# Kernel tuning notes

Measured on AMD Instinct MI355X. Metric: run time of the kernel, lower is better.

Reference implementation:

```python
import jax, jax.numpy as jnp
import numpy as np

L = 5        # num_layers
DIM = 128    # data dim
SPLIT = DIM // 2   # 64
H = 64       # hidden_dim (fixed in AffineCouplingLayer)
OUT = DIM - SPLIT  # 64
B = 262144   # batch


def setup_inputs() -> dict:
    key = jax.random.key(0)
    ks = jax.random.split(key, 13)

    def p(k, shape, fan_in):
        return jax.random.normal(k, shape, jnp.float32) * (1.0 / np.sqrt(fan_in))

    inp = {
        "x": jax.random.normal(ks[0], (B, DIM), jnp.float32),
        # s_net params, stacked over layers. Linear stored as [in, out] (y = x @ W + b)
        "s_W1": p(ks[1], (L, SPLIT, H), SPLIT), "s_b1": jnp.zeros((L, H), jnp.float32),
        "s_W2": p(ks[2], (L, H, H), H),         "s_b2": jnp.zeros((L, H), jnp.float32),
        "s_W3": p(ks[3], (L, H, OUT), H),       "s_b3": jnp.zeros((L, OUT), jnp.float32),
        # t_net params
        "t_W1": p(ks[4], (L, SPLIT, H), SPLIT), "t_b1": jnp.zeros((L, H), jnp.float32),
        "t_W2": p(ks[5], (L, H, H), H),         "t_b2": jnp.zeros((L, H), jnp.float32),
        "t_W3": p(ks[6], (L, H, OUT), H),       "t_b3": jnp.zeros((L, OUT), jnp.float32),
    }
    return inp


def _mlp(x0, W1, b1, W2, b2, W3, b3):
    # 3-layer MLP with LeakyReLU(0.01) between layers (torch default slope)
    h = jax.nn.leaky_relu(x0 @ W1 + b1, 0.01)
    h = jax.nn.leaky_relu(h @ W2 + b2, 0.01)
    return h @ W3 + b3


def reference(x, s_W1, s_b1, s_W2, s_b2, s_W3, s_b3,
              t_W1, t_b1, t_W2, t_b2, t_W3, t_b3):
    x0 = x[:, :SPLIT]          # never changes across layers (matches source)
    x1 = x[:, SPLIT:]
    log_det = jnp.zeros(x.shape[0], x.dtype)
    for l in range(L):
        s = jnp.tanh(_mlp(x0, s_W1[l], s_b1[l], s_W2[l], s_b2[l], s_W3[l], s_b3[l]))
        t = _mlp(x0, t_W1[l], t_b1[l], t_W2[l], t_b2[l], t_W3[l], t_b3[l])
        x1 = x1 * jnp.exp(s) + t
        log_det = log_det + jnp.sum(s, axis=1)
    z = jnp.concatenate([x0, x1], axis=1)
    return z, log_det
```

## Files before the change

### kernel.cpp

```cpp
#include <hip/hip_runtime.h>

typedef __fp16 f16;
typedef __fp16 f16x2 __attribute__((ext_vector_type(2)));
typedef __fp16 f16x8 __attribute__((ext_vector_type(8)));
typedef float f32x4 __attribute__((ext_vector_type(4)));
typedef float f32x16 __attribute__((ext_vector_type(16)));

__device__ __forceinline__ unsigned pkrtz(float a, float b) {
    f16x2 r = __builtin_amdgcn_cvt_pkrtz(a, b);
    return __builtin_bit_cast(unsigned, r);
}

__device__ __forceinline__ f16x8 pack4(unsigned a, unsigned b, unsigned c, unsigned d) {
    union { unsigned u[4]; f16x8 v; } r;
    r.u[0] = a; r.u[1] = b; r.u[2] = c; r.u[3] = d;
    return r.v;
}

__global__ __launch_bounds__(512) void pack_w(
    const float* __restrict__ sW1, const float* __restrict__ sW2, const float* __restrict__ sW3,
    const float* __restrict__ tW1, const float* __restrict__ tW2, const float* __restrict__ tW3,
    f16* __restrict__ wp) {
    int mat = blockIdx.x;
    int layer = mat / 6;
    int rem = mat % 6;
    int fi = threadIdx.x >> 6;
    int lane = threadIdx.x & 63;
    int tile = fi >> 2, kt = fi & 3;
    int h = lane >> 5;
    int m = (lane & 31) + 32 * tile;
    const float* Wt[6] = {sW1, sW2, sW3, tW1, tW2, tW3};
    const float* W = Wt[rem] + layer * 4096;
    f16x8 v;
#pragma unroll
    for (int e = 0; e < 8; ++e) {
        int k = 16 * kt + 4 * h + (e & 3) + ((e >> 2) << 3);
        v[e] = (f16)W[k * 64 + m];
    }
    *(f16x8*)(wp + ((size_t)mat * 8 + fi) * 512 + lane * 8) = v;
}

__global__ __launch_bounds__(512) void pack_b(
    const float* __restrict__ sb1, const float* __restrict__ sb2, const float* __restrict__ sb3,
    const float* __restrict__ tb1, const float* __restrict__ tb2, const float* __restrict__ tb3,
    float* __restrict__ wb) {
    int i = blockIdx.x * 512 + threadIdx.x;
    if (i >= 1920) return;
    int l = i / 384, r = i % 384, mat = r / 64, j = r % 64;
    const float* B[6] = {sb1, sb2, sb3, tb1, tb2, tb3};
    wb[l * 384 + mat * 64 + j] = B[mat][l * 64 + j];
}

__device__ __forceinline__ void bias_init(const float* bias, int h, f32x16 c[2]) {
#pragma unroll
    for (int t = 0; t < 2; ++t) {
#pragma unroll
        for (int r4 = 0; r4 < 4; ++r4) {
            f32x4 bb = *(const f32x4*)(bias + 32 * t + 8 * r4 + 4 * h);
            c[t][4 * r4 + 0] = bb[0];
            c[t][4 * r4 + 1] = bb[1];
            c[t][4 * r4 + 2] = bb[2];
            c[t][4 * r4 + 3] = bb[3];
        }
    }
}

__device__ __forceinline__ void gemm1(const f16* w, const f16x8 in[4],
                                      const float* bias, int lane, f32x16 c[2]) {
    const int h = (lane >> 5) & 1;
    bias_init(bias, h, c);
#pragma unroll
    for (int mt = 0; mt < 2; ++mt) {
#pragma unroll
        for (int kt = 0; kt < 4; ++kt) {
            f16x8 wf = *(const f16x8*)(w + (mt * 4 + kt) * 512 + lane * 8);
            c[mt] = __builtin_amdgcn_mfma_f32_32x32x16_f16(wf, in[kt], c[mt], 0, 0, 0);
        }
    }
}

__device__ __forceinline__ void relu_pack(const f32x16 c[2], f16x8 o[4]) {
    const f16 hc = (f16)0.01f;
    const f16x8 c001 = {hc, hc, hc, hc, hc, hc, hc, hc};
#pragma unroll
    for (int kt = 0; kt < 4; ++kt) {
        const int tl = kt >> 1;
        const int base = 8 * (kt & 1);
        f16x8 v = pack4(pkrtz(c[tl][base + 0], c[tl][base + 1]),
                        pkrtz(c[tl][base + 2], c[tl][base + 3]),
                        pkrtz(c[tl][base + 4], c[tl][base + 5]),
                        pkrtz(c[tl][base + 6], c[tl][base + 7]));
        o[kt] = __builtin_elementwise_max(v, v * c001);
    }
}

__device__ __forceinline__ void mlp3(const f16* w, const f16x8 x0f[4],
                                     int lane, f32x16 out[2]) {
    const float* bias = (const float*)(w + 12288);
    f32x16 c1[2];
    gemm1(w, x0f, bias, lane, c1);
    f16x8 h1[4];
    relu_pack(c1, h1);
    f32x16 c2[2];
    gemm1(w + 4096, h1, bias + 64, lane, c2);
    f16x8 h2[4];
    relu_pack(c2, h2);
    gemm1(w + 8192, h2, bias + 128, lane, out);
}

#define SLOT 12672

__global__ __launch_bounds__(512, 2)
void flow_main(const float* __restrict__ x, const f16* __restrict__ wp,
               float* __restrict__ out, int nrows) {
    __shared__ f16 wl[SLOT];
    const int tid = threadIdx.x;
    const int lane = tid & 63;
    const int wv = tid >> 6;
    const int h = lane >> 5;
    const int n = (blockIdx.x * 8 + wv) * 32 + (lane & 31);
    const float* xr = x + (size_t)n * 128;
    float* zr = out + (size_t)n * 128;
    const float* wbias_g = (const float*)((const char*)wp + 491520);

    f32x4 stg0, stg1, stg2;
    f32x4 stgb = {0.f, 0.f, 0.f, 0.f};

    {
        const f32x4* src = (const f32x4*)wp;
        stg0 = src[tid]; stg1 = src[tid + 512]; stg2 = src[tid + 1024];
        f32x4* dst = (f32x4*)wl;
        dst[tid] = stg0; dst[tid + 512] = stg1; dst[tid + 1024] = stg2;
        if (tid < 48) {
            stgb = ((const f32x4*)wbias_g)[tid];
            ((f32x4*)(wl + 12288))[tid] = stgb;
        }
    }

    f16x8 x0f[4];
#pragma unroll
    for (int kt = 0; kt < 4; ++kt) {
        f32x4 a = *(const f32x4*)(xr + 16 * kt + 4 * h);
        f32x4 b = *(const f32x4*)(xr + 16 * kt + 8 + 4 * h);
        *(f32x4*)(zr + 16 * kt + 4 * h) = a;
        *(f32x4*)(zr + 16 * kt + 8 + 4 * h) = b;
        x0f[kt] = pack4(pkrtz(a[0], a[1]), pkrtz(a[2], a[3]), pkrtz(b[0], b[1]), pkrtz(b[2], b[3]));
    }

    f16x8 x1h[4];
#pragma unroll
    for (int i = 0; i < 4; ++i) {
        const int t = i >> 1, q = i & 1;
        f32x4 a = *(const f32x4*)(xr + 64 + 32 * t + 16 * q + 4 * h);
        f32x4 b = *(const f32x4*)(xr + 64 + 32 * t + 16 * q + 8 + 4 * h);
        x1h[i] = pack4(pkrtz(a[0], a[1]), pkrtz(a[2], a[3]),
                       pkrtz(b[0], b[1]), pkrtz(b[2], b[3]));
    }

    __syncthreads();

    float ld = 0.f;
#pragma unroll 1
    for (int l = 0; l < 5; ++l) {
        {
            const f32x4* src = (const f32x4*)(wp + (size_t)l * 24576 + 12288);
            stg0 = src[tid]; stg1 = src[tid + 512]; stg2 = src[tid + 1024];
            if (tid < 48) stgb = ((const f32x4*)(wbias_g + l * 384 + 192))[tid];
        }

        f32x16 cs[2];
        mlp3(wl, x0f, lane, cs);

#pragma unroll
        for (int i = 0; i < 4; ++i) {
            const int t = i >> 1, q = i & 1;
            f16x8 xo = x1h[i];
            float nf[8];
#pragma unroll
            for (int e = 0; e < 8; ++e) {
                float y = cs[t][8 * q + e];
                float u = __builtin_amdgcn_exp2f(2.8853900817779268f * y);
                float rc = __builtin_amdgcn_rcpf(u + 1.f);
                float s = fmaf(-2.f, rc, 1.f);
                ld += s;
                float ef = __builtin_amdgcn_exp2f(fmaf(-2.8853900817779268f, rc, 1.4426950408889634f));
                nf[e] = (float)xo[e] * ef;
            }
            x1h[i] = pack4(pkrtz(nf[0], nf[1]), pkrtz(nf[2], nf[3]),
                           pkrtz(nf[4], nf[5]), pkrtz(nf[6], nf[7]));
        }

        __syncthreads();
        {
            f32x4* dst = (f32x4*)wl;
            dst[tid] = stg0; dst[tid + 512] = stg1; dst[tid + 1024] = stg2;
            if (tid < 48) ((f32x4*)(wl + 12288))[tid] = stgb;
        }
        __syncthreads();

        if (l < 4) {
            const f32x4* src = (const f32x4*)(wp + (size_t)(l + 1) * 24576);
            stg0 = src[tid]; stg1 = src[tid + 512]; stg2 = src[tid + 1024];
            if (tid < 48) stgb = ((const f32x4*)(wbias_g + (l + 1) * 384))[tid];
        }

        f32x16 ct[2];
        mlp3(wl, x0f, lane, ct);

#pragma unroll
        for (int i = 0; i < 4; ++i) {
            const int t = i >> 1, q = i & 1;
            f16x8 xo = x1h[i];
            float nf[8];
#pragma unroll
            for (int e = 0; e < 8; ++e)
                nf[e] = (float)xo[e] + ct[t][8 * q + e];
            x1h[i] = pack4(pkrtz(nf[0], nf[1]), pkrtz(nf[2], nf[3]),
                           pkrtz(nf[4], nf[5]), pkrtz(nf[6], nf[7]));
        }

        if (l < 4) {
            __syncthreads();
            {
                f32x4* dst = (f32x4*)wl;
                dst[tid] = stg0; dst[tid + 512] = stg1; dst[tid + 1024] = stg2;
                if (tid < 48) ((f32x4*)(wl + 12288))[tid] = stgb;
            }
            __syncthreads();
        }
    }

#pragma unroll
    for (int i = 0; i < 4; ++i) {
        const int t = i >> 1, q = i & 1;
        f16x8 v = x1h[i];
        f32x4 a = {(float)v[0], (float)v[1], (float)v[2], (float)v[3]};
        f32x4 b = {(float)v[4], (float)v[5], (float)v[6], (float)v[7]};
        *(f32x4*)(zr + 64 + 32 * t + 16 * q + 4 * h) = a;
        *(f32x4*)(zr + 64 + 32 * t + 16 * q + 8 + 4 * h) = b;
    }

    float tot = ld + __shfl_xor(ld, 32);
    if (h == 0) out[(size_t)nrows * 128 + n] = tot;
}

extern "C" void kernel_launch(void* const* d_in, const int* in_sizes, int n_in,
                              void* d_out, int out_size, void* d_ws, size_t ws_size,
                              hipStream_t stream) {
    const float* x   = (const float*)d_in[0];
    const float* sW1 = (const float*)d_in[1];
    const float* sb1 = (const float*)d_in[2];
    const float* sW2 = (const float*)d_in[3];
    const float* sb2 = (const float*)d_in[4];
    const float* sW3 = (const float*)d_in[5];
    const float* sb3 = (const float*)d_in[6];
    const float* tW1 = (const float*)d_in[7];
    const float* tb1 = (const float*)d_in[8];
    const float* tW2 = (const float*)d_in[9];
    const float* tb2 = (const float*)d_in[10];
    const float* tW3 = (const float*)d_in[11];
    const float* tb3 = (const float*)d_in[12];

    f16* wp = (f16*)d_ws;
    float* wb = (float*)((char*)d_ws + 491520);
    int nrows = in_sizes[0] / 128;

    pack_w<<<30, 512, 0, stream>>>(sW1, sW2, sW3, tW1, tW2, tW3, wp);
    pack_b<<<4, 512, 0, stream>>>(sb1, sb2, sb3, tb1, tb2, tb3, wb);
    flow_main<<<nrows / 256, 512, 0, stream>>>(x, wp, (float*)d_out, nrows);
}
```

Baseline: 139.2 us.

## Double-buffer weight slots in LDS using direct global-to-LDS loads

Register-staged weight copies are replaced by asynchronous global_load_lds transfers into two LDS slots. The next MLP's weights stream into one slot while the current MLP reads the other, which drops one barrier pair per layer half and frees the staging registers. MFMA loops are also wrapped in s_setprio so matrix work gets issue priority. The cost is double the LDS footprint per block, which could limit occupancy, plus reliance on the compiler placing the right waits before each barrier.

```diff
diff --git a/kernel.cpp b/kernel.cpp
--- a/kernel.cpp
+++ b/kernel.cpp
@@ -15,6 +15,12 @@
     union { unsigned u[4]; f16x8 v; } r;
     r.u[0] = a; r.u[1] = b; r.u[2] = c; r.u[3] = d;
     return r.v;
+}
+
+__device__ __forceinline__ void glds16(const void* g, void* l) {
+    __builtin_amdgcn_global_load_lds(
+        (const __attribute__((address_space(1))) unsigned*)g,
+        (__attribute__((address_space(3))) unsigned*)l, 16, 0, 0);
 }
 
 __global__ __launch_bounds__(512) void pack_w(
@@ -69,6 +75,7 @@
                                       const float* bias, int lane, f32x16 c[2]) {
     const int h = (lane >> 5) & 1;
     bias_init(bias, h, c);
+    __builtin_amdgcn_s_setprio(1);
 #pragma unroll
     for (int mt = 0; mt < 2; ++mt) {
 #pragma unroll
@@ -77,6 +84,7 @@
             c[mt] = __builtin_amdgcn_mfma_f32_32x32x16_f16(wf, in[kt], c[mt], 0, 0, 0);
         }
     }
+    __builtin_amdgcn_s_setprio(0);
 }
 
 __device__ __forceinline__ void relu_pack(const f32x16 c[2], f16x8 o[4]) {
@@ -108,12 +116,12 @@
     gemm1(w + 8192, h2, bias + 128, lane, out);
 }
 
-#define SLOT 12672
+#define SLOTB 25344
 
 __global__ __launch_bounds__(512, 2)
 void flow_main(const float* __restrict__ x, const f16* __restrict__ wp,
                float* __restrict__ out, int nrows) {
-    __shared__ f16 wl[SLOT];
+    __shared__ char wl[2 * SLOTB];
     const int tid = threadIdx.x;
     const int lane = tid & 63;
     const int wv = tid >> 6;
@@ -121,21 +129,21 @@
     const int n = (blockIdx.x * 8 + wv) * 32 + (lane & 31);
     const float* xr = x + (size_t)n * 128;
     float* zr = out + (size_t)n * 128;
-    const float* wbias_g = (const float*)((const char*)wp + 491520);
-
-    f32x4 stg0, stg1, stg2;
-    f32x4 stgb = {0.f, 0.f, 0.f, 0.f};
-
-    {
-        const f32x4* src = (const f32x4*)wp;
-        stg0 = src[tid]; stg1 = src[tid + 512]; stg2 = src[tid + 1024];
-        f32x4* dst = (f32x4*)wl;
-        dst[tid] = stg0; dst[tid + 512] = stg1; dst[tid + 1024] = stg2;
-        if (tid < 48) {
-            stgb = ((const f32x4*)wbias_g)[tid];
-            ((f32x4*)(wl + 12288))[tid] = stgb;
-        }
-    }
+    const char* wp_b = (const char*)wp;
+    const char* wb_b = (const char*)wp + 491520;
+
+    auto stage = [&](int pi, char* slot) {
+#pragma unroll
+        for (int j = 0; j < 3; ++j) {
+            const int chunk = wv + j * 8;
+            glds16(wp_b + (size_t)pi * 24576 + chunk * 1024 + lane * 16,
+                   slot + chunk * 1024);
+        }
+        if (wv == 0 && lane < 48)
+            glds16(wb_b + (size_t)pi * 768 + lane * 16, slot + 24576);
+    };
+
+    stage(0, wl);
 
     f16x8 x0f[4];
 #pragma unroll
@@ -162,14 +170,10 @@
     float ld = 0.f;
 #pragma unroll 1
     for (int l = 0; l < 5; ++l) {
-        {
-            const f32x4* src = (const f32x4*)(wp + (size_t)l * 24576 + 12288);
-            stg0 = src[tid]; stg1 = src[tid + 512]; stg2 = src[tid + 1024];
-            if (tid < 48) stgb = ((const f32x4*)(wbias_g + l * 384 + 192))[tid];
-        }
+        stage(2 * l + 1, wl + SLOTB);
 
         f32x16 cs[2];
-        mlp3(wl, x0f, lane, cs);
+        mlp3((const f16*)wl, x0f, lane, cs);
 
 #pragma unroll
         for (int i = 0; i < 4; ++i) {
@@ -191,21 +195,11 @@
         }
 
         __syncthreads();
-        {
-            f32x4* dst = (f32x4*)wl;
-            dst[tid] = stg0; dst[tid + 512] = stg1; dst[tid + 1024] = stg2;
-            if (tid < 48) ((f32x4*)(wl + 12288))[tid] = stgb;
-        }
-        __syncthreads();
-
-        if (l < 4) {
-            const f32x4* src = (const f32x4*)(wp + (size_t)(l + 1) * 24576);
-            stg0 = src[tid]; stg1 = src[tid + 512]; stg2 = src[tid + 1024];
-            if (tid < 48) stgb = ((const f32x4*)(wbias_g + (l + 1) * 384))[tid];
-        }
+
+        if (l < 4) stage(2 * l + 2, wl);
 
         f32x16 ct[2];
-        mlp3(wl, x0f, lane, ct);
+        mlp3((const f16*)(wl + SLOTB), x0f, lane, ct);
 
 #pragma unroll
         for (int i = 0; i < 4; ++i) {
@@ -219,15 +213,7 @@
                            pkrtz(nf[4], nf[5]), pkrtz(nf[6], nf[7]));
         }
 
-        if (l < 4) {
-            __syncthreads();
-            {
-                f32x4* dst = (f32x4*)wl;
-                dst[tid] = stg0; dst[tid + 512] = stg1; dst[tid + 1024] = stg2;
-                if (tid < 48) ((f32x4*)(wl + 12288))[tid] = stgb;
-            }
-            __syncthreads();
-        }
+        __syncthreads();
     }
 
 #pragma unroll
```

New measurement: 117.2 us. 15.8% less time.
